# Kernel tuning notes

Hardware: AMD Instinct MI355X
Metric: run time of the kernel (lower is better)

The kernel has to match this reference:

```python
import jax, jax.numpy as jnp
import numpy as np

B, C, RES, N_ANGLES = 32, 16, 128, 64


def setup_inputs() -> dict:
    key = jax.random.key(0)
    k1, k2, k3 = jax.random.split(key, 3)
    x = jax.random.normal(k1, (B, C, RES, RES), dtype=jnp.float32)
    # torch-radon setup: angles = np.linspace(0, 2*pi, 64)
    angles = jnp.linspace(0.0, 2.0 * np.pi, N_ANGLES).astype(jnp.float32)
    # Conv2d(16, 1, 1) params (kaiming-ish scale)
    conv_w = jax.random.normal(k2, (1, C, 1, 1), dtype=jnp.float32) * (1.0 / np.sqrt(C))
    conv_b = jax.random.normal(k3, (1,), dtype=jnp.float32) * 0.01
    return {"x": x, "angles": angles, "conv_w": conv_w, "conv_b": conv_b}


def _radon(x, angles):
    # x: (B, C, H, W) -> sinogram (B, C, n_angles, det_count)
    H = x.shape[-2]
    W = x.shape[-1]
    center = (H - 1) / 2.0
    # detector positions s and ray-integration positions t, in pixel units, centered
    coords = jnp.arange(H, dtype=jnp.float32) - center  # (RES,)

    def proj_one(carry, theta):
        c, s = jnp.cos(theta), jnp.sin(theta)
        # rotated sampling grid: (D, T) = (detector, along-ray)
        xs = coords[:, None] * c - coords[None, :] * s + center
        ys = coords[:, None] * s + coords[None, :] * c + center
        x0 = jnp.floor(xs)
        y0 = jnp.floor(ys)
        wx = xs - x0  # bilinear weights
        wy = ys - y0
        x0i = x0.astype(jnp.int32)
        y0i = y0.astype(jnp.int32)

        def g(yi, xi):
            # zero-padded gather: (B, C, D, T)
            valid = ((yi >= 0) & (yi < H) & (xi >= 0) & (xi < W)).astype(x.dtype)
            v = x[:, :, jnp.clip(yi, 0, H - 1), jnp.clip(xi, 0, W - 1)]
            return v * valid

        val = (g(y0i, x0i) * ((1.0 - wy) * (1.0 - wx))
               + g(y0i, x0i + 1) * ((1.0 - wy) * wx)
               + g(y0i + 1, x0i) * (wy * (1.0 - wx))
               + g(y0i + 1, x0i + 1) * (wy * wx))
        # line integral: sum along the ray (T axis) -> (B, C, D)
        return carry, val.sum(axis=-1)

    _, sino = jax.lax.scan(proj_one, 0, angles)  # (A, B, C, D)
    return jnp.transpose(sino, (1, 2, 0, 3))      # (B, C, A, D)


def reference(x, angles, conv_w, conv_b):
    sino = _radon(x, angles)  # (B, C, A, D)
    # 1x1 conv: contract channel dim
    out = jnp.einsum('bcad,oc->boad', sino, conv_w[:, :, 0, 0])
    return out + conv_b[None, :, None, None]
```

## Files before the change

kernel.cpp:

```cpp
#include <hip/hip_runtime.h>


#define B_    32
#define C_    16
#define RES   128
#define NA    64
#define SLDS  133
#define ROWS  132
#define NELEM (ROWS * SLDS)
#define NPAD  18432
#define NPAIR 16

typedef _Float16 half2v __attribute__((ext_vector_type(2)));

__global__ __launch_bounds__(256) void chanpack(const float* __restrict__ x,
                                                const float* __restrict__ w,
                                                uint2* __restrict__ pk) {
    const int blk = blockIdx.x;
    const int p   = blk >> 7;
    const int q   = blk & 127;
    const int t   = threadIdx.x;
    const int u   = t >> 7;
    const int m   = t & 127;

    __shared__ float rowbuf[2][130];

    float wr[C_];
#pragma unroll
    for (int c = 0; c < C_; ++c) wr[c] = w[c];

    const float* xb = x + ((size_t)(2 * p + u) * C_) * (RES * RES) + q * RES + m;
    float acc = 0.f;
#pragma unroll
    for (int c = 0; c < C_; ++c) acc = fmaf(wr[c], xb[c * (RES * RES)], acc);

    rowbuf[u][m + 1] = acc;
    if (m == 0) { rowbuf[u][0] = 0.f; rowbuf[u][129] = 0.f; }
    __syncthreads();

    uint2* dst = pk + (size_t)p * NPAD + (q + 2) * SLDS;
    if (t < SLDS) {
        int c = t;
        uint2 v = make_uint2(0u, 0u);
        if (c >= 1 && c <= 129) {
            v.x = __builtin_bit_cast(unsigned int,
                      __builtin_amdgcn_cvt_pkrtz(rowbuf[0][c - 1], rowbuf[0][c]));
            v.y = __builtin_bit_cast(unsigned int,
                      __builtin_amdgcn_cvt_pkrtz(rowbuf[1][c - 1], rowbuf[1][c]));
        }
        dst[c] = v;
    }

    if (q == 0) {
        uint2* base = pk + (size_t)p * NPAD;
        const uint2 z = make_uint2(0u, 0u);
        for (int k = t; k < 2 * SLDS; k += 256) {
            base[k] = z;
            base[130 * SLDS + k] = z;
        }
        for (int k = t; k < NPAD - NELEM; k += 256)
            base[NELEM + k] = z;
    }
}

__global__ __launch_bounds__(512) void radon_k(const uint2* __restrict__ pk,
                                               const float* __restrict__ angles,
                                               const float* __restrict__ bias,
                                               float* __restrict__ out) {
    __shared__ uint2 lds[NPAD];
    const int bid = blockIdx.x;
    const int p   = bid >> 4;
    const int grp = bid & 15;
    const int t   = threadIdx.x;

    {
        const uint4* src = (const uint4*)(pk + (size_t)p * NPAD);
        uint4*       dst = (uint4*)lds;
#pragma unroll
        for (int k = 0; k < 18; ++k) dst[k * 512 + t] = src[k * 512 + t];
    }
    __syncthreads();

    const int a = (t >> 7) * 16 + grp;
    const int i = t & 127;
    float th = angles[a];
    float s, c;
    __sincosf(th, &s, &c);

    const float ci = (float)i - 63.5f;
    const float Xb = fmaf(ci, c, fmaf(63.5f, s, 65.5f));
    const float Yb = fmaf(ci, s, fmaf(-63.5f, c, 65.5f));
    const float ns = -s;

    float acc00 = 0.f, acc01 = 0.f, acc10 = 0.f, acc11 = 0.f;
#pragma unroll 8
    for (int j = 0; j < RES; ++j) {
        float jf = (float)j;
        float X  = fmaf(jf, ns, Xb);
        float Y  = fmaf(jf, c,  Yb);
        float fx = floorf(X), fy = floorf(Y);
        float wx = X - fx,    wy = Y - fy;
        float gx = fminf(fmaxf(fx, 0.f), 130.f);
        float gy = fminf(fmaxf(fy, 0.f), 130.f);
        int addr = (int)fmaf(gy, (float)SLDS, gx);
        uint2 q0 = lds[addr];
        uint2 q1 = lds[addr + SLDS];
        float un = 1.f - wx;
        float A0 = 1.f - wy;
        half2v wa = __builtin_bit_cast(half2v, __builtin_amdgcn_cvt_pkrtz(A0 * un, A0 * wx));
        half2v wb = __builtin_bit_cast(half2v, __builtin_amdgcn_cvt_pkrtz(wy * un, wy * wx));
        acc00 = __builtin_amdgcn_fdot2(__builtin_bit_cast(half2v, q0.x), wa, acc00, false);
        acc10 = __builtin_amdgcn_fdot2(__builtin_bit_cast(half2v, q0.y), wa, acc10, false);
        acc01 = __builtin_amdgcn_fdot2(__builtin_bit_cast(half2v, q1.x), wb, acc01, false);
        acc11 = __builtin_amdgcn_fdot2(__builtin_bit_cast(half2v, q1.y), wb, acc11, false);
    }

    float bv = bias[0];
    out[(2 * p)     * (NA * RES) + a * RES + i] = (acc00 + acc01) + bv;
    out[(2 * p + 1) * (NA * RES) + a * RES + i] = (acc10 + acc11) + bv;
}

extern "C" void kernel_launch(void* const* d_in, const int* in_sizes, int n_in,
                              void* d_out, int out_size, void* d_ws, size_t ws_size,
                              hipStream_t stream) {
    const float* x      = (const float*)d_in[0];
    const float* angles = (const float*)d_in[1];
    const float* w      = (const float*)d_in[2];
    const float* bias   = (const float*)d_in[3];
    float* out = (float*)d_out;

    uint2* pk = (uint2*)d_ws;

    chanpack<<<dim3(NPAIR * RES), dim3(256), 0, stream>>>(x, w, pk);
    radon_k<<<dim3(NPAIR * 16), dim3(512), 0, stream>>>(pk, angles, bias, out);
}
```

Before: 96.85 us.

## Split ray integration across two blocks with atomic accumulation and halve LDS footprint

Changes the packed layout from two-pixel-pair uint2 to a single half2 per pixel (batch pair), halving LDS to about 72KB so two blocks fit per CU. Each ray is now split into two halves handled by separate blocks, doubling the grid, with the results combined through atomicAdd into a zeroed output. Bilinear taps now use four scalar LDS reads and fp32 FMAs instead of packed fdot2. This adds a memset and atomics, plus more LDS loads per sample, in exchange for higher occupancy and parallelism.

```diff
diff --git a/kernel.cpp b/kernel.cpp
--- a/kernel.cpp
+++ b/kernel.cpp
@@ -8,14 +8,14 @@
 #define SLDS  133
 #define ROWS  132
 #define NELEM (ROWS * SLDS)
-#define NPAD  18432
+#define NPADE 18432
 #define NPAIR 16
 
 typedef _Float16 half2v __attribute__((ext_vector_type(2)));
 
 __global__ __launch_bounds__(256) void chanpack(const float* __restrict__ x,
                                                 const float* __restrict__ w,
-                                                uint2* __restrict__ pk) {
+                                                unsigned int* __restrict__ pk) {
     const int blk = blockIdx.x;
     const int p   = blk >> 7;
     const int q   = blk & 127;
@@ -23,7 +23,7 @@
     const int u   = t >> 7;
     const int m   = t & 127;
 
-    __shared__ float rowbuf[2][130];
+    __shared__ float rowbuf[2][128];
 
     float wr[C_];
 #pragma unroll
@@ -34,50 +34,46 @@
 #pragma unroll
     for (int c = 0; c < C_; ++c) acc = fmaf(wr[c], xb[c * (RES * RES)], acc);
 
-    rowbuf[u][m + 1] = acc;
-    if (m == 0) { rowbuf[u][0] = 0.f; rowbuf[u][129] = 0.f; }
+    rowbuf[u][m] = acc;
     __syncthreads();
 
-    uint2* dst = pk + (size_t)p * NPAD + (q + 2) * SLDS;
+    unsigned int* dst = pk + (size_t)p * NPADE + (q + 2) * SLDS;
     if (t < SLDS) {
         int c = t;
-        uint2 v = make_uint2(0u, 0u);
-        if (c >= 1 && c <= 129) {
-            v.x = __builtin_bit_cast(unsigned int,
-                      __builtin_amdgcn_cvt_pkrtz(rowbuf[0][c - 1], rowbuf[0][c]));
-            v.y = __builtin_bit_cast(unsigned int,
-                      __builtin_amdgcn_cvt_pkrtz(rowbuf[1][c - 1], rowbuf[1][c]));
-        }
+        unsigned int v = 0u;
+        if (c >= 2 && c <= 129)
+            v = __builtin_bit_cast(unsigned int,
+                    __builtin_amdgcn_cvt_pkrtz(rowbuf[0][c - 2], rowbuf[1][c - 2]));
         dst[c] = v;
     }
 
     if (q == 0) {
-        uint2* base = pk + (size_t)p * NPAD;
-        const uint2 z = make_uint2(0u, 0u);
+        unsigned int* base = pk + (size_t)p * NPADE;
         for (int k = t; k < 2 * SLDS; k += 256) {
-            base[k] = z;
-            base[130 * SLDS + k] = z;
+            base[k] = 0u;
+            base[130 * SLDS + k] = 0u;
         }
-        for (int k = t; k < NPAD - NELEM; k += 256)
-            base[NELEM + k] = z;
+        for (int k = t; k < NPADE - NELEM; k += 256)
+            base[NELEM + k] = 0u;
     }
 }
 
-__global__ __launch_bounds__(512) void radon_k(const uint2* __restrict__ pk,
-                                               const float* __restrict__ angles,
-                                               const float* __restrict__ bias,
-                                               float* __restrict__ out) {
-    __shared__ uint2 lds[NPAD];
+__global__ __launch_bounds__(512, 2) void radon_k(const unsigned int* __restrict__ pk,
+                                                  const float* __restrict__ angles,
+                                                  const float* __restrict__ bias,
+                                                  float* __restrict__ out) {
+    __shared__ unsigned int lds[NPADE];
     const int bid = blockIdx.x;
-    const int p   = bid >> 4;
-    const int grp = bid & 15;
+    const int h   = bid & 1;
+    const int grp = (bid >> 1) & 15;
+    const int p   = bid >> 5;
     const int t   = threadIdx.x;
 
     {
-        const uint4* src = (const uint4*)(pk + (size_t)p * NPAD);
+        const uint4* src = (const uint4*)(pk + (size_t)p * NPADE);
         uint4*       dst = (uint4*)lds;
 #pragma unroll
-        for (int k = 0; k < 18; ++k) dst[k * 512 + t] = src[k * 512 + t];
+        for (int k = 0; k < 9; ++k) dst[k * 512 + t] = src[k * 512 + t];
     }
     __syncthreads();
 
@@ -88,13 +84,14 @@
     __sincosf(th, &s, &c);
 
     const float ci = (float)i - 63.5f;
-    const float Xb = fmaf(ci, c, fmaf(63.5f, s, 65.5f));
-    const float Yb = fmaf(ci, s, fmaf(-63.5f, c, 65.5f));
+    const float j0 = (float)(h * 64);
+    const float Xb = fmaf(ci, c, fmaf(63.5f - j0, s, 65.5f));
+    const float Yb = fmaf(ci, s, fmaf(j0 - 63.5f, c, 65.5f));
     const float ns = -s;
 
-    float acc00 = 0.f, acc01 = 0.f, acc10 = 0.f, acc11 = 0.f;
+    float acc0 = 0.f, acc1 = 0.f;
 #pragma unroll 8
-    for (int j = 0; j < RES; ++j) {
+    for (int j = 0; j < 64; ++j) {
         float jf = (float)j;
         float X  = fmaf(jf, ns, Xb);
         float Y  = fmaf(jf, c,  Yb);
@@ -103,21 +100,26 @@
         float gx = fminf(fmaxf(fx, 0.f), 130.f);
         float gy = fminf(fmaxf(fy, 0.f), 130.f);
         int addr = (int)fmaf(gy, (float)SLDS, gx);
-        uint2 q0 = lds[addr];
-        uint2 q1 = lds[addr + SLDS];
+        half2v q00 = __builtin_bit_cast(half2v, lds[addr]);
+        half2v q01 = __builtin_bit_cast(half2v, lds[addr + 1]);
+        half2v q10 = __builtin_bit_cast(half2v, lds[addr + SLDS]);
+        half2v q11 = __builtin_bit_cast(half2v, lds[addr + SLDS + 1]);
         float un = 1.f - wx;
         float A0 = 1.f - wy;
-        half2v wa = __builtin_bit_cast(half2v, __builtin_amdgcn_cvt_pkrtz(A0 * un, A0 * wx));
-        half2v wb = __builtin_bit_cast(half2v, __builtin_amdgcn_cvt_pkrtz(wy * un, wy * wx));
-        acc00 = __builtin_amdgcn_fdot2(__builtin_bit_cast(half2v, q0.x), wa, acc00, false);
-        acc10 = __builtin_amdgcn_fdot2(__builtin_bit_cast(half2v, q0.y), wa, acc10, false);
-        acc01 = __builtin_amdgcn_fdot2(__builtin_bit_cast(half2v, q1.x), wb, acc01, false);
-        acc11 = __builtin_amdgcn_fdot2(__builtin_bit_cast(half2v, q1.y), wb, acc11, false);
+        float w00 = A0 * un, w01 = A0 * wx, w10 = wy * un, w11 = wy * wx;
+        acc0 = fmaf((float)q00.x, w00, acc0);
+        acc1 = fmaf((float)q00.y, w00, acc1);
+        acc0 = fmaf((float)q01.x, w01, acc0);
+        acc1 = fmaf((float)q01.y, w01, acc1);
+        acc0 = fmaf((float)q10.x, w10, acc0);
+        acc1 = fmaf((float)q10.y, w10, acc1);
+        acc0 = fmaf((float)q11.x, w11, acc0);
+        acc1 = fmaf((float)q11.y, w11, acc1);
     }
 
-    float bv = bias[0];
-    out[(2 * p)     * (NA * RES) + a * RES + i] = (acc00 + acc01) + bv;
-    out[(2 * p + 1) * (NA * RES) + a * RES + i] = (acc10 + acc11) + bv;
+    float bv = (h == 0) ? bias[0] : 0.f;
+    atomicAdd(&out[(2 * p)     * (NA * RES) + a * RES + i], acc0 + bv);
+    atomicAdd(&out[(2 * p + 1) * (NA * RES) + a * RES + i], acc1 + bv);
 }
 
 extern "C" void kernel_launch(void* const* d_in, const int* in_sizes, int n_in,
@@ -129,8 +131,9 @@
     const float* bias   = (const float*)d_in[3];
     float* out = (float*)d_out;
 
-    uint2* pk = (uint2*)d_ws;
+    unsigned int* pk = (unsigned int*)d_ws;
 
+    hipMemsetAsync(out, 0, (size_t)out_size * sizeof(float), stream);
     chanpack<<<dim3(NPAIR * RES), dim3(256), 0, stream>>>(x, w, pk);
-    radon_k<<<dim3(NPAIR * 16), dim3(512), 0, stream>>>(pk, angles, bias, out);
+    radon_k<<<dim3(NPAIR * 16 * 2), dim3(512), 0, stream>>>(pk, angles, bias, out);
 }
```

After: 97.71 us. About the same (+0.9%).
